# Optimization experiments

Hardware: AMD Instinct MI355X
Metric: run time of the kernel (lower is better)

The kernel has to match this reference:

```python
import jax, jax.numpy as jnp
import numpy as np

B, N, D = 8, 2048, 128
NEG = -9.0e15


def setup_inputs() -> dict:
    key = jax.random.key(0)
    ks = jax.random.split(key, 7)
    x = jax.random.normal(ks[0], (B, N, D), dtype=jnp.float32)
    # sparse-ish binary adjacency with self loops, stored dense as float
    adj = (jax.random.uniform(ks[1], (B, N, N)) < 0.1).astype(jnp.float32)
    adj = jnp.maximum(adj, jnp.eye(N, dtype=jnp.float32)[None])
    s = 1.0 / np.sqrt(D)
    W_w = jax.random.uniform(ks[2], (D, D), minval=-s, maxval=s, dtype=jnp.float32)
    W_b = jax.random.uniform(ks[3], (D,), minval=-s, maxval=s, dtype=jnp.float32)
    A = jnp.zeros((D, D), dtype=jnp.float32) + 0.01 * jax.random.normal(ks[4], (D, D), dtype=jnp.float32)
    s2 = 1.0 / np.sqrt(2 * D)
    gate_w = jax.random.uniform(ks[5], (1, 2 * D), minval=-s2, maxval=s2, dtype=jnp.float32)
    gate_b = jax.random.uniform(ks[6], (1,), minval=-s2, maxval=s2, dtype=jnp.float32)
    return {"x": x, "adj": adj, "W_w": W_w, "W_b": W_b, "A": A,
            "gate_w": gate_w, "gate_b": gate_b}


def reference(x, adj, W_w, W_b, A, gate_w, gate_b):
    # h = W(x): [B,N,D]
    h = jnp.einsum('bnf,df->bnd', x, W_w) + W_b
    # e[b,j,k] = (h A)[b,j,:] . h[b,k,:], then symmetrize
    hA = jnp.einsum('bnd,de->bne', h, A)
    e = jnp.einsum('bjl,bkl->bjk', hA, h)
    e = e + jnp.swapaxes(e, 1, 2)
    att = jnp.where(adj > 0, e, jnp.full_like(e, NEG))
    # NOTE: torch code softmaxes over dim=1 (the j axis)
    att = jax.nn.softmax(att, axis=1)
    att = att * adj
    h_prime = jax.nn.relu(jnp.einsum('bij,bjk->bik', att, h))
    gate_in = jnp.concatenate([x, h_prime], axis=-1)  # [B,N,2D]
    coeff = jax.nn.sigmoid(jnp.einsum('bnc,oc->bno', gate_in, gate_w) + gate_b)  # [B,N,1]
    return coeff * x + (1.0 - coeff) * h_prime
```

## Files before the change

### kernel.cpp

```cpp
#include <hip/hip_runtime.h>


#define B_ 8
#define N_ 2048
#define D_ 128

typedef __attribute__((ext_vector_type(8))) short short8;
typedef __attribute__((ext_vector_type(4))) float f32x4;
typedef __attribute__((ext_vector_type(2))) float f32x2;

#define GLL(gp, lp) __builtin_amdgcn_global_load_lds( \
    (__attribute__((address_space(1))) const unsigned int*)(gp), \
    (__attribute__((address_space(3))) unsigned int*)(lp), 16, 0, 0)

static __device__ __forceinline__ unsigned short f2bf(float f) {
  union { float f; unsigned int u; } v; v.f = f;
  unsigned int r = v.u + 0x7fffu + ((v.u >> 16) & 1u);
  return (unsigned short)(r >> 16);
}
static __device__ __forceinline__ float bf2f(unsigned short u) {
  union { unsigned int u; float f; } v; v.u = ((unsigned int)u) << 16;
  return v.f;
}

#define CAT_OFF  ((size_t)0)
#define VT_OFF   ((size_t)8388608)
#define PUN_OFF  ((size_t)12582912)
#define S_OFF    ((size_t)79691776)
#define WB_OFF   ((size_t)79757312)
#define AT_OFF   ((size_t)79790080)

__global__ __launch_bounds__(256) void k_cvt(const float* __restrict__ W,
                                             const float* __restrict__ A,
                                             unsigned short* __restrict__ Wb1,
                                             unsigned short* __restrict__ Abt) {
  int i = blockIdx.x * 256 + threadIdx.x;
  Wb1[i] = f2bf(W[i]);
  Abt[(i & 127) * 128 + (i >> 7)] = f2bf(A[i]);
}

__global__ __launch_bounds__(256) void k1(const float* __restrict__ x,
                                          const unsigned short* __restrict__ Wb1,
                                          const float* __restrict__ Wbias,
                                          const unsigned short* __restrict__ Abt,
                                          unsigned short* __restrict__ cat) {
  __shared__ unsigned short hsm[4][16][136];
  __shared__ unsigned short hasm[4][16][136];
  const int t = threadIdx.x, w = t >> 6, lane = t & 63;
  const int q = lane >> 4, l15 = lane & 15;
  const size_t r0 = (size_t)blockIdx.x * 64 + w * 16;

  f32x4 acc[8];
#pragma unroll
  for (int dg = 0; dg < 8; dg++) acc[dg] = (f32x4){0.f, 0.f, 0.f, 0.f};
#pragma unroll
  for (int k = 0; k < 4; k++) {
    const float* xp = x + (r0 + l15) * 128 + k * 32 + q * 8;
    f32x4 xa = *(const f32x4*)xp;
    f32x4 xb = *(const f32x4*)(xp + 4);
    short8 af;
#pragma unroll
    for (int e = 0; e < 4; e++) { af[e] = (short)f2bf(xa[e]); af[4 + e] = (short)f2bf(xb[e]); }
#pragma unroll
    for (int dg = 0; dg < 8; dg++) {
      short8 bf = *(const short8*)(Wb1 + (dg * 16 + l15) * 128 + k * 32 + q * 8);
      acc[dg] = __builtin_amdgcn_mfma_f32_16x16x32_bf16(af, bf, acc[dg], 0, 0, 0);
    }
  }
#pragma unroll
  for (int dg = 0; dg < 8; dg++) {
    float bias = Wbias[dg * 16 + l15];
#pragma unroll
    for (int r = 0; r < 4; r++)
      hsm[w][q * 4 + r][dg * 16 + l15] = f2bf(acc[dg][r] + bias);
  }
  __syncthreads();
  f32x4 acc2[8];
#pragma unroll
  for (int dg = 0; dg < 8; dg++) acc2[dg] = (f32x4){0.f, 0.f, 0.f, 0.f};
#pragma unroll
  for (int k = 0; k < 4; k++) {
    short8 af = *(short8*)&hsm[w][l15][k * 32 + q * 8];
#pragma unroll
    for (int dg = 0; dg < 8; dg++) {
      short8 bf = *(const short8*)(Abt + (dg * 16 + l15) * 128 + k * 32 + q * 8);
      acc2[dg] = __builtin_amdgcn_mfma_f32_16x16x32_bf16(af, bf, acc2[dg], 0, 0, 0);
    }
  }
#pragma unroll
  for (int dg = 0; dg < 8; dg++)
#pragma unroll
    for (int r = 0; r < 4; r++)
      hasm[w][q * 4 + r][dg * 16 + l15] = f2bf(acc2[dg][r]);
  __syncthreads();
#pragma unroll
  for (int it = 0; it < 8; it++) {
    int idx = it * 64 + lane;
    int row = idx >> 5, c = idx & 31;
    short8 v = (c < 16) ? *(short8*)&hasm[w][row][c * 8]
                        : *(short8*)&hsm[w][row][(c - 16) * 8];
    *(short8*)(cat + ((r0 + row) << 8) + c * 8) = v;
  }
}

__global__ __launch_bounds__(256, 2) void k2(const unsigned short* __restrict__ cat,
                                             const float* __restrict__ adj,
                                             unsigned short* __restrict__ pun,
                                             float* __restrict__ s_out) {
  __shared__ unsigned short cj[2][64 * 256];
  const int t = threadIdx.x, w = t >> 6, lane = t & 63;
  const int q = lane >> 4, l15 = lane & 15;
  const int b = blockIdx.z;
  const int kbase = blockIdx.x * 128;
  const int j0b = blockIdx.y * 512;
  const size_t bN = (size_t)b * N_;
  const unsigned short* catp = cat + (bN << 8);
  const int kc = kbase + w * 32;
  short8 brg[2][8];
#pragma unroll
  for (int p = 0; p < 2; p++) {
    int krow = kc + 2 * l15 + p;
#pragma unroll
    for (int m = 0; m < 8; m++)
      brg[p][m] = *(const short8*)(catp + (((size_t)krow) << 8) +
                                   ((((m * 4 + q) + 16) & 31) * 8));
  }
  float acc0 = 0.f, acc1 = 0.f;

#define K2_STAGE(tt, bufi) do { \
    const int j0_ = j0b + (tt) * 64; \
    _Pragma("unroll") \
    for (int it = 0; it < 8; it++) { \
      int sI = it * 256 + t; \
      int row = sI >> 5, c = sI & 31; \
      GLL(catp + (((size_t)(j0_ + row)) << 8) + (c ^ (row & 7)) * 8, \
          (char*)cj[bufi] + sI * 16); \
    } } while (0)

#define K2_ADJ(tt, av) do { \
    const int j0_ = j0b + (tt) * 64; \
    _Pragma("unroll") \
    for (int js = 0; js < 4; js++) \
      _Pragma("unroll") \
      for (int r = 0; r < 4; r++) { \
        int jrow = j0_ + js * 16 + q * 4 + r; \
        av[js][r] = *(const f32x2*)(adj + (((size_t)(bN + jrow)) << 11) + kc + 2 * l15); \
      } } while (0)

#define K2_COMPUTE(tt, bufi, av) do { \
    const int j0_ = j0b + (tt) * 64; \
    _Pragma("unroll") \
    for (int jsub = 0; jsub < 4; jsub++) { \
      const int row = jsub * 16 + l15; \
      short8 afr[8]; \
      _Pragma("unroll") \
      for (int m = 0; m < 8; m++) \
        afr[m] = *(short8*)(cj[bufi] + row * 256 + (((m * 4 + q) ^ (l15 & 7)) * 8)); \
      f32x4 e0 = {0.f, 0.f, 0.f, 0.f}, e1 = {0.f, 0.f, 0.f, 0.f}; \
      _Pragma("unroll") \
      for (int m = 0; m < 8; m++) { \
        e0 = __builtin_amdgcn_mfma_f32_16x16x32_bf16(afr[m], brg[0][m], e0, 0, 0, 0); \
        e1 = __builtin_amdgcn_mfma_f32_16x16x32_bf16(afr[m], brg[1][m], e1, 0, 0, 0); \
      } \
      _Pragma("unroll") \
      for (int r = 0; r < 4; r++) { \
        int jrow = j0_ + jsub * 16 + q * 4 + r; \
        float x0 = (av[jsub][r][0] > 0.f) ? __expf(fminf(e0[r], 60.f)) : 0.f; \
        float x1 = (av[jsub][r][1] > 0.f) ? __expf(fminf(e1[r], 60.f)) : 0.f; \
        acc0 += x0; acc1 += x1; \
        unsigned int pk = (unsigned int)f2bf(x0) | ((unsigned int)f2bf(x1) << 16); \
        *(unsigned int*)(pun + ((bN + jrow) << 11) + kc + 2 * l15) = pk; \
      } \
    } } while (0)

  f32x2 avA[4][4], avB[4][4];
  K2_STAGE(0, 0);
  K2_ADJ(0, avA);
  __syncthreads();
#pragma unroll
  for (int tp = 0; tp < 4; tp++) {
    K2_STAGE(2 * tp + 1, 1);
    K2_ADJ(2 * tp + 1, avB);
    K2_COMPUTE(2 * tp, 0, avA);
    __syncthreads();
    if (2 * tp + 2 < 8) {
      K2_STAGE(2 * tp + 2, 0);
      K2_ADJ(2 * tp + 2, avA);
    }
    K2_COMPUTE(2 * tp + 1, 1, avB);
    __syncthreads();
  }
#undef K2_STAGE
#undef K2_ADJ
#undef K2_COMPUTE

  acc0 += __shfl_xor(acc0, 16, 64); acc0 += __shfl_xor(acc0, 32, 64);
  acc1 += __shfl_xor(acc1, 16, 64); acc1 += __shfl_xor(acc1, 32, 64);
  if (lane < 16) {
    atomicAdd(&s_out[bN + kc + 2 * lane], acc0);
    atomicAdd(&s_out[bN + kc + 2 * lane + 1], acc1);
  }
}

__global__ __launch_bounds__(256) void k1v(const unsigned short* __restrict__ cat,
                                           const float* __restrict__ s,
                                           unsigned short* __restrict__ vt) {
  __shared__ unsigned short tile[64][136];
  __shared__ float rsv[64];
  const int t = threadIdx.x;
  const int b = blockIdx.y;
  const int nbase = blockIdx.x * 64;
  if (t < 64) rsv[t] = 1.f / s[(size_t)b * N_ + nbase + t];
#pragma unroll
  for (int k = 0; k < 4; k++) {
    int sI = t + 256 * k;
    int row = sI >> 4, part = sI & 15;
    *(short8*)&tile[row][part * 8] =
        *(const short8*)(cat + (((size_t)(b * N_ + nbase + row)) << 8) + 128 + part * 8);
  }
  __syncthreads();
#pragma unroll
  for (int k = 0; k < 4; k++) {
    int sI = t + 256 * k;
    int dd = sI >> 3, part = sI & 7;
    unsigned short tmp[8];
#pragma unroll
    for (int j = 0; j < 8; j++) {
      int jj = part * 8 + j;
      tmp[j] = f2bf(bf2f(tile[jj][dd]) * rsv[jj]);
    }
    *(short8*)(vt + (((size_t)(b * 128 + dd)) << 11) + nbase + part * 8) = *(short8*)tmp;
  }
}

__global__ __launch_bounds__(256) void k3(const unsigned short* __restrict__ pun,
                                          const unsigned short* __restrict__ vt,
                                          const float* __restrict__ x,
                                          const float* __restrict__ gw,
                                          const float* __restrict__ gb,
                                          float* __restrict__ out) {
  __shared__ char smem[40960];
  const int t = threadIdx.x, w = t >> 6, lane = t & 63;
  const int q = lane >> 4, l15 = lane & 15;
  const int b = blockIdx.y, i0 = blockIdx.x * 32;
  const size_t bN = (size_t)b * N_;
  unsigned short* pa = (unsigned short*)smem;
  unsigned short* vb = (unsigned short*)(smem + 8192);

  f32x4 acc[2][2];
#pragma unroll
  for (int ih = 0; ih < 2; ih++)
#pragma unroll
    for (int dh = 0; dh < 2; dh++) acc[ih][dh] = (f32x4){0.f, 0.f, 0.f, 0.f};

  for (int jt = 0; jt < N_ / 128; jt++) {
    const int j0 = jt * 128;
#pragma unroll
    for (int it = 0; it < 10; it++) {
      int sI = it * 256 + t;
      const unsigned short* g;
      if (sI < 512) {
        int row = sI >> 4, c = sI & 15;
        g = pun + (((size_t)(bN + i0 + row)) << 11) + j0 + ((c ^ (row & 7)) * 8);
      } else {
        int s2 = sI - 512;
        int dd = s2 >> 4, c = s2 & 15;
        g = vt + (((size_t)(b * 128 + dd)) << 11) + j0 + ((c ^ (dd & 7)) * 8);
      }
      GLL(g, smem + sI * 16);
    }
    __syncthreads();
#pragma unroll
    for (int ks = 0; ks < 4; ks++) {
      short8 af[2], bf[2];
#pragma unroll
      for (int ih = 0; ih < 2; ih++) {
        int m = ih * 16 + l15;
        af[ih] = *(short8*)(pa + m * 128 + (((ks * 4 + q) ^ (m & 7)) * 8));
      }
#pragma unroll
      for (int dh = 0; dh < 2; dh++) {
        int d = w * 32 + dh * 16 + l15;
        bf[dh] = *(short8*)(vb + d * 128 + (((ks * 4 + q) ^ (d & 7)) * 8));
      }
      acc[0][0] = __builtin_amdgcn_mfma_f32_16x16x32_bf16(af[0], bf[0], acc[0][0], 0, 0, 0);
      acc[0][1] = __builtin_amdgcn_mfma_f32_16x16x32_bf16(af[0], bf[1], acc[0][1], 0, 0, 0);
      acc[1][0] = __builtin_amdgcn_mfma_f32_16x16x32_bf16(af[1], bf[0], acc[1][0], 0, 0, 0);
      acc[1][1] = __builtin_amdgcn_mfma_f32_16x16x32_bf16(af[1], bf[1], acc[1][1], 0, 0, 0);
    }
    __syncthreads();
  }
  float* hs = (float*)smem;
  float* co = (float*)(smem + 16896);
#pragma unroll
  for (int ih = 0; ih < 2; ih++)
#pragma unroll
    for (int dh = 0; dh < 2; dh++)
#pragma unroll
      for (int r = 0; r < 4; r++) {
        int row = ih * 16 + q * 4 + r;
        int d = w * 32 + dh * 16 + l15;
        hs[row * 132 + d] = fmaxf(acc[ih][dh][r], 0.f);
      }
  __syncthreads();
  {
    int grow = t >> 3, sub = t & 7;
    const float* xr = x + (((size_t)(bN + i0 + grow)) << 7);
    float z = 0.f;
#pragma unroll
    for (int k = 0; k < 16; k++) {
      int dd = sub + 8 * k;
      z += gw[dd] * xr[dd] + gw[128 + dd] * hs[grow * 132 + dd];
    }
    z += __shfl_xor(z, 1, 64);
    z += __shfl_xor(z, 2, 64);
    z += __shfl_xor(z, 4, 64);
    if (sub == 0) co[grow] = 1.f / (1.f + __expf(-(z + gb[0])));
  }
  __syncthreads();
#pragma unroll
  for (int kk = 0; kk < 4; kk++) {
    int id = kk * 256 + t;
    int row = id >> 5, c4 = id & 31;
    size_t g = (((size_t)(bN + i0 + row)) << 7) + c4 * 4;
    f32x4 xv = *(const f32x4*)(x + g);
    f32x4 hv = *(const f32x4*)(hs + row * 132 + c4 * 4);
    float cf = co[row];
    f32x4 o;
#pragma unroll
    for (int e = 0; e < 4; e++) o[e] = cf * xv[e] + (1.f - cf) * hv[e];
    *(f32x4*)(out + g) = o;
  }
}

extern "C" void kernel_launch(void* const* d_in, const int* in_sizes, int n_in,
                              void* d_out, int out_size, void* d_ws, size_t ws_size,
                              hipStream_t stream) {
  const float* x   = (const float*)d_in[0];
  const float* adj = (const float*)d_in[1];
  const float* Ww  = (const float*)d_in[2];
  const float* Wb  = (const float*)d_in[3];
  const float* A   = (const float*)d_in[4];
  const float* gw  = (const float*)d_in[5];
  const float* gb  = (const float*)d_in[6];
  float* out = (float*)d_out;
  char* ws = (char*)d_ws;

  unsigned short* cat = (unsigned short*)(ws + CAT_OFF);
  unsigned short* vt  = (unsigned short*)(ws + VT_OFF);
  unsigned short* pun = (unsigned short*)(ws + PUN_OFF);
  float* s  = (float*)(ws + S_OFF);
  unsigned short* Wb1 = (unsigned short*)(ws + WB_OFF);
  unsigned short* Abt = (unsigned short*)(ws + AT_OFF);

  hipMemsetAsync(s, 0, (size_t)B_ * N_ * sizeof(float), stream);
  k_cvt<<<64, 256, 0, stream>>>(Ww, A, Wb1, Abt);
  k1<<<(B_ * N_) / 64, 256, 0, stream>>>(x, Wb1, Wb, Abt, cat);
  k2<<<dim3(16, 4, B_), 256, 0, stream>>>(cat, adj, pun, s);
  k1v<<<dim3(N_ / 64, B_), 256, 0, stream>>>(cat, s, vt);
  k3<<<dim3(N_ / 32, B_), 256, 0, stream>>>(pun, vt, x, gw, gb, out);
}
```

Measured before the change: 265.4 us.

## Double-buffer k3 LDS tiles and use partial vmcnt waits to overlap loads

```diff
diff --git a/kernel.cpp b/kernel.cpp
--- a/kernel.cpp
+++ b/kernel.cpp
@@ -12,6 +12,9 @@
 #define GLL(gp, lp) __builtin_amdgcn_global_load_lds( \
     (__attribute__((address_space(1))) const unsigned int*)(gp), \
     (__attribute__((address_space(3))) unsigned int*)(lp), 16, 0, 0)
+
+#define VMW(N) asm volatile("s_waitcnt vmcnt(" #N ")" ::: "memory")
+#define BARRIER() __builtin_amdgcn_s_barrier()
 
 static __device__ __forceinline__ unsigned short f2bf(float f) {
   union { float f; unsigned int u; } v; v.f = f;
@@ -176,19 +179,24 @@
   f32x2 avA[4][4], avB[4][4];
   K2_STAGE(0, 0);
   K2_ADJ(0, avA);
-  __syncthreads();
 #pragma unroll
   for (int tp = 0; tp < 4; tp++) {
     K2_STAGE(2 * tp + 1, 1);
     K2_ADJ(2 * tp + 1, avB);
+    VMW(40);
+    BARRIER();
     K2_COMPUTE(2 * tp, 0, avA);
-    __syncthreads();
+    BARRIER();
     if (2 * tp + 2 < 8) {
       K2_STAGE(2 * tp + 2, 0);
       K2_ADJ(2 * tp + 2, avA);
-    }
+      VMW(40);
+    } else {
+      VMW(16);
+    }
+    BARRIER();
     K2_COMPUTE(2 * tp + 1, 1, avB);
-    __syncthreads();
+    BARRIER();
   }
 #undef K2_STAGE
 #undef K2_ADJ
@@ -239,13 +247,11 @@
                                           const float* __restrict__ gw,
                                           const float* __restrict__ gb,
                                           float* __restrict__ out) {
-  __shared__ char smem[40960];
+  __shared__ char smem[2][40960];
   const int t = threadIdx.x, w = t >> 6, lane = t & 63;
   const int q = lane >> 4, l15 = lane & 15;
   const int b = blockIdx.y, i0 = blockIdx.x * 32;
   const size_t bN = (size_t)b * N_;
-  unsigned short* pa = (unsigned short*)smem;
-  unsigned short* vb = (unsigned short*)(smem + 8192);
 
   f32x4 acc[2][2];
 #pragma unroll
@@ -253,45 +259,62 @@
 #pragma unroll
     for (int dh = 0; dh < 2; dh++) acc[ih][dh] = (f32x4){0.f, 0.f, 0.f, 0.f};
 
-  for (int jt = 0; jt < N_ / 128; jt++) {
-    const int j0 = jt * 128;
-#pragma unroll
-    for (int it = 0; it < 10; it++) {
-      int sI = it * 256 + t;
-      const unsigned short* g;
-      if (sI < 512) {
-        int row = sI >> 4, c = sI & 15;
-        g = pun + (((size_t)(bN + i0 + row)) << 11) + j0 + ((c ^ (row & 7)) * 8);
-      } else {
-        int s2 = sI - 512;
-        int dd = s2 >> 4, c = s2 & 15;
-        g = vt + (((size_t)(b * 128 + dd)) << 11) + j0 + ((c ^ (dd & 7)) * 8);
-      }
-      GLL(g, smem + sI * 16);
-    }
-    __syncthreads();
-#pragma unroll
-    for (int ks = 0; ks < 4; ks++) {
-      short8 af[2], bf[2];
-#pragma unroll
-      for (int ih = 0; ih < 2; ih++) {
-        int m = ih * 16 + l15;
-        af[ih] = *(short8*)(pa + m * 128 + (((ks * 4 + q) ^ (m & 7)) * 8));
-      }
-#pragma unroll
-      for (int dh = 0; dh < 2; dh++) {
-        int d = w * 32 + dh * 16 + l15;
-        bf[dh] = *(short8*)(vb + d * 128 + (((ks * 4 + q) ^ (d & 7)) * 8));
-      }
-      acc[0][0] = __builtin_amdgcn_mfma_f32_16x16x32_bf16(af[0], bf[0], acc[0][0], 0, 0, 0);
-      acc[0][1] = __builtin_amdgcn_mfma_f32_16x16x32_bf16(af[0], bf[1], acc[0][1], 0, 0, 0);
-      acc[1][0] = __builtin_amdgcn_mfma_f32_16x16x32_bf16(af[1], bf[0], acc[1][0], 0, 0, 0);
-      acc[1][1] = __builtin_amdgcn_mfma_f32_16x16x32_bf16(af[1], bf[1], acc[1][1], 0, 0, 0);
-    }
-    __syncthreads();
-  }
-  float* hs = (float*)smem;
-  float* co = (float*)(smem + 16896);
+#define K3_STAGE(jtv, bufi) do { \
+    const int j0_ = (jtv) * 128; \
+    _Pragma("unroll") \
+    for (int it = 0; it < 10; it++) { \
+      int sI = it * 256 + t; \
+      const unsigned short* g; \
+      if (sI < 512) { \
+        int row = sI >> 4, c = sI & 15; \
+        g = pun + (((size_t)(bN + i0 + row)) << 11) + j0_ + ((c ^ (row & 7)) * 8); \
+      } else { \
+        int s2 = sI - 512; \
+        int dd = s2 >> 4, c = s2 & 15; \
+        g = vt + (((size_t)(b * 128 + dd)) << 11) + j0_ + ((c ^ (dd & 7)) * 8); \
+      } \
+      GLL(g, smem[bufi] + sI * 16); \
+    } } while (0)
+
+#define K3_COMPUTE(bufi) do { \
+    unsigned short* pa = (unsigned short*)smem[bufi]; \
+    unsigned short* vb = (unsigned short*)(smem[bufi] + 8192); \
+    _Pragma("unroll") \
+    for (int ks = 0; ks < 4; ks++) { \
+      short8 af[2], bf[2]; \
+      _Pragma("unroll") \
+      for (int ih = 0; ih < 2; ih++) { \
+        int m = ih * 16 + l15; \
+        af[ih] = *(short8*)(pa + m * 128 + (((ks * 4 + q) ^ (m & 7)) * 8)); \
+      } \
+      _Pragma("unroll") \
+      for (int dh = 0; dh < 2; dh++) { \
+        int d = w * 32 + dh * 16 + l15; \
+        bf[dh] = *(short8*)(vb + d * 128 + (((ks * 4 + q) ^ (d & 7)) * 8)); \
+      } \
+      acc[0][0] = __builtin_amdgcn_mfma_f32_16x16x32_bf16(af[0], bf[0], acc[0][0], 0, 0, 0); \
+      acc[0][1] = __builtin_amdgcn_mfma_f32_16x16x32_bf16(af[0], bf[1], acc[0][1], 0, 0, 0); \
+      acc[1][0] = __builtin_amdgcn_mfma_f32_16x16x32_bf16(af[1], bf[0], acc[1][0], 0, 0, 0); \
+      acc[1][1] = __builtin_amdgcn_mfma_f32_16x16x32_bf16(af[1], bf[1], acc[1][1], 0, 0, 0); \
+    } } while (0)
+
+  K3_STAGE(0, 0);
+  for (int jt = 0; jt < 15; jt++) {
+    K3_STAGE(jt + 1, (jt + 1) & 1);
+    asm volatile("s_waitcnt vmcnt(10)" ::: "memory");
+    BARRIER();
+    K3_COMPUTE(jt & 1);
+    BARRIER();
+  }
+  asm volatile("s_waitcnt vmcnt(0)" ::: "memory");
+  BARRIER();
+  K3_COMPUTE(1);
+  __syncthreads();
+#undef K3_STAGE
+#undef K3_COMPUTE
+
+  float* hs = (float*)smem[0];
+  float* co = (float*)(smem[0] + 16896);
 #pragma unroll
   for (int ih = 0; ih < 2; ih++)
 #pragma unroll
```

After: 266.3 us. Within noise of the previous version (+0.3%).
